# Kernel optimization log

Hardware: AMD Instinct MI355X
Metric: run time of the kernel (lower is better)

Reference implementation:

```python
import jax, jax.numpy as jnp
import numpy as np
from jax import lax

D_IN, HIDDEN, B, T = 64, 512, 256, 256


def _lstm_layer(x, W_ih, W_hh, b_ih, b_hh):
    """PyTorch-convention LSTM layer. x: [B, T, in]. Returns (ys [B,T,H], h_last [B,H]).
    Gate order i, f, g, o; gates = x W_ih^T + h W_hh^T + b_ih + b_hh."""
    Bb = x.shape[0]
    H = W_hh.shape[1]
    # precompute input projection for all timesteps: [T, B, 4H]
    xg = jnp.einsum('bti,gi->tbg', x, W_ih) + (b_ih + b_hh)
    h0 = jnp.zeros((Bb, H), dtype=x.dtype)
    c0 = jnp.zeros((Bb, H), dtype=x.dtype)

    def step(carry, xg_t):
        h, c = carry
        gates = xg_t + h @ W_hh.T  # [B, 4H]
        i, f, g, o = jnp.split(gates, 4, axis=-1)
        i = jax.nn.sigmoid(i)
        f = jax.nn.sigmoid(f)
        g = jnp.tanh(g)
        o = jax.nn.sigmoid(o)
        c = f * c + i * g
        h = o * jnp.tanh(c)
        return (h, c), h

    (h_last, _), ys = lax.scan(step, (h0, c0), xg)
    return ys.transpose(1, 0, 2), h_last


def setup_inputs() -> dict:
    key = jax.random.key(0)
    ks = jax.random.split(key, 12)
    s0 = 1.0 / np.sqrt(HIDDEN)  # PyTorch default init scale
    u = lambda k, shp: jax.random.uniform(k, shp, jnp.float32, -s0, s0)
    return {
        'x': jax.random.normal(ks[0], (B, T, D_IN), jnp.float32),
        'W_ih0': u(ks[1], (4 * HIDDEN, D_IN)),
        'W_hh0': u(ks[2], (4 * HIDDEN, HIDDEN)),
        'b_ih0': u(ks[3], (4 * HIDDEN,)),
        'b_hh0': u(ks[4], (4 * HIDDEN,)),
        'W_ih1': u(ks[5], (4 * HIDDEN, HIDDEN)),
        'W_hh1': u(ks[6], (4 * HIDDEN, HIDDEN)),
        'b_ih1': u(ks[7], (4 * HIDDEN,)),
        'b_hh1': u(ks[8], (4 * HIDDEN,)),
        'head_w': u(ks[9], (1, HIDDEN)),
        'head_b': u(ks[10], (1,)),
    }


def reference(x, W_ih0, W_hh0, b_ih0, b_hh0, W_ih1, W_hh1, b_ih1, b_hh1, head_w, head_b):
    ys0, _ = _lstm_layer(x, W_ih0, W_hh0, b_ih0, b_hh0)          # [B, T, H]
    _, h_last = _lstm_layer(ys0, W_ih1, W_hh1, b_ih1, b_hh1)    # only last step used
    out = h_last @ head_w.T + head_b                              # [B, 1]
    return out[:, 0]                                              # squeeze(-1) -> [B]
```

## Files before the change

kernel.cpp:

```cpp
#include <hip/hip_runtime.h>

#define HID 512
#define NB  256
#define TT  256
#define DIN 64
#define HBUF 131072
#define SLOT_SH HBUF
#define NSLOT 8

typedef __attribute__((ext_vector_type(8))) short short8;
typedef __attribute__((ext_vector_type(4))) float f32x4;

__device__ __forceinline__ unsigned short f2bf(float f) {
    unsigned int u = __float_as_uint(f);
    u += 0x7FFF + ((u >> 16) & 1);
    return (unsigned short)(u >> 16);
}
__device__ __forceinline__ float bf2f(unsigned short h) {
    return __uint_as_float(((unsigned int)h) << 16);
}

__device__ __forceinline__ float fsig(float x) {
    return __builtin_amdgcn_rcpf(1.f + __expf(-x));
}
__device__ __forceinline__ float ftanh(float x) {
    return 1.f - 2.f * __builtin_amdgcn_rcpf(1.f + __expf(2.f * x));
}

__device__ __forceinline__ void st_u32_llc(unsigned* p, unsigned v) {
    asm volatile("global_store_dword %0, %1, off sc0 sc1" :: "v"(p), "v"(v) : "memory");
}
__device__ __forceinline__ unsigned ld_u32_llc(const unsigned* p) {
    unsigned v;
    asm volatile("global_load_dword %0, %1, off sc0 sc1\n\ts_waitcnt vmcnt(0)"
                 : "=v"(v) : "v"(p) : "memory");
    return v;
}

#define MFMA1(acc, a, b) acc = __builtin_amdgcn_mfma_f32_16x16x32_bf16(a, b, acc, 0, 0, 0)

#define SW0_F 36
#define SW1_F 64
#define SW0_N (SW0_F * 512)
#define SW1_N (SW1_F * 512)
#define LDS_BYTES ((SW0_N + SW1_N) * 2)

__device__ __forceinline__ void store_h_pair(unsigned short* buf, size_t hoff,
                                             unsigned short v, int l) {
    unsigned int hv = (unsigned int)v;
    unsigned int up = __shfl_down(hv, 1);
    if ((l & 1) == 0)
        st_u32_llc((unsigned*)(buf + hoff), hv | (up << 16));
}

__device__ __forceinline__ void flag_wait(unsigned* fset, int target) {
    if (threadIdx.x < 64) {
        unsigned* p = fset + threadIdx.x;
        while ((int)ld_u32_llc(p) < target) __builtin_amdgcn_s_sleep(1);
    }
    __syncthreads();
}

__device__ __forceinline__ void orbit_transpose(f32x4& v, int m) {
    { float a = (m & 1) ? v[0] : v[1]; float b = __shfl_xor(a, 4); if (m & 1) v[0] = b; else v[1] = b; }
    { float a = (m & 1) ? v[2] : v[3]; float b = __shfl_xor(a, 4); if (m & 1) v[2] = b; else v[3] = b; }
    { float a = (m & 2) ? v[0] : v[2]; float b = __shfl_xor(a, 8); if (m & 2) v[0] = b; else v[2] = b; }
    { float a = (m & 2) ? v[1] : v[3]; float b = __shfl_xor(a, 8); if (m & 2) v[1] = b; else v[3] = b; }
}

__global__ __launch_bounds__(512, 2) void lstm_persistent(
    const float* __restrict__ x,
    const float* __restrict__ Wih0, const float* __restrict__ Whh0,
    const float* __restrict__ bih0, const float* __restrict__ bhh0,
    const float* __restrict__ Wih1, const float* __restrict__ Whh1,
    const float* __restrict__ bih1, const float* __restrict__ bhh1,
    const float* __restrict__ headw, const float* __restrict__ headb,
    unsigned short* h0base, unsigned short* h1base,
    unsigned* gf, float* __restrict__ out)
{
    extern __shared__ unsigned short lds[];
    unsigned short* sW0 = lds;
    unsigned short* sW1 = lds + SW0_N;

    const int tid = threadIdx.x;
    const int l   = tid & 63;
    const int w   = tid >> 6;
    const int bt  = w >> 1;
    const int bf  = w & 1;
    const int bid = blockIdx.x;
    const int gq  = bid & 3;
    const int jb  = bid >> 2;

    unsigned* f0g = gf + gq * 64;
    unsigned* f1g = gf + 256 + gq * 64;

    const int r16 = l & 15;
    const int ko  = (l >> 4) * 8;
    {
        const int nrow = (r16 >> 2) * HID + jb * 8 + (r16 & 3);
        for (int fi = w; fi < SW0_F; fi += 8) {
            const int kt = fi >> 1, bf_ = fi & 1;
            const int n = nrow + bf_ * 4;
            const float* src = (kt < 2) ? (Wih0 + (size_t)n * DIN + kt * 32 + ko)
                                        : (Whh0 + (size_t)n * HID + (kt - 2) * 32 + ko);
            float v[8];
            *(float4*)&v[0] = *(const float4*)src;
            *(float4*)&v[4] = *(const float4*)(src + 4);
            union { unsigned short u[8]; uint4 q; } pb;
            #pragma unroll
            for (int e = 0; e < 8; ++e) pb.u[e] = f2bf(v[e]);
            *(uint4*)&sW0[fi * 512 + l * 8] = pb.q;
        }
        for (int fi = w; fi < SW1_F; fi += 8) {
            const int kt = fi >> 1, bf_ = fi & 1;
            const int n = nrow + bf_ * 4;
            const float* src = (kt < 16) ? (Wih1 + (size_t)n * HID + kt * 32 + ko)
                                         : (Whh1 + (size_t)n * HID + (kt - 16) * 32 + ko);
            float v[8];
            *(float4*)&v[0] = *(const float4*)src;
            *(float4*)&v[4] = *(const float4*)(src + 4);
            union { unsigned short u[8]; uint4 q; } pb;
            #pragma unroll
            for (int e = 0; e < 8; ++e) pb.u[e] = f2bf(v[e]);
            *(uint4*)&sW1[fi * 512 + l * 8] = pb.q;
        }
    }

    float bias0[4], bias1[4];
    #pragma unroll
    for (int gi = 0; gi < 4; ++gi) {
        const int nn = gi * HID + jb * 8 + bf * 4 + (l & 3);
        bias0[gi] = bih0[nn] + bhh0[nn];
        bias1[gi] = bih1[nn] + bhh1[nn];
    }
    float c0 = 0.f, c1 = 0.f;

    const int m      = (l >> 2) & 3;
    const int b_in   = (l >> 4) * 4 + m;
    const int b_glob = gq * 64 + bt * 16 + b_in;
    const int j_glob = jb * 8 + bf * 4 + (l & 3);
    const size_t hoff = ((((size_t)(b_glob >> 4)) * 16 + (j_glob >> 5)) * 64
                         + ((b_glob & 15) | (((j_glob >> 3) & 3) << 4))) * 8 + (j_glob & 7);
    const int btg = gq * 4 + bt;

    const int xrow = gq * 64 + bt * 16 + (l & 15);
    float xv0[8], xv1[8];
    {
        const float* s0 = x + ((size_t)xrow * TT + 0) * DIN + ko;
        *(float4*)&xv0[0] = *(const float4*)s0;
        *(float4*)&xv0[4] = *(const float4*)(s0 + 4);
        *(float4*)&xv1[0] = *(const float4*)(s0 + 32);
        *(float4*)&xv1[4] = *(const float4*)(s0 + 36);
    }

    __syncthreads();

    const short8 bx0 = *(const short8*)&sW0[(0 * 2 + bf) * 512 + l * 8];
    const short8 bx1 = *(const short8*)&sW0[(1 * 2 + bf) * 512 + l * 8];

    for (int it = 0; it <= TT; ++it) {
        flag_wait(f0g, it);

        const unsigned short* h0c = h0base + (size_t)((it + 7) & 7) * SLOT_SH;
        unsigned short* h0n       = h0base + (size_t)(it & 7) * SLOT_SH;
        const unsigned short* h1c = h1base + (size_t)((it + 6) & 7) * SLOT_SH;
        unsigned short* h1n       = h1base + (size_t)((it + 7) & 7) * SLOT_SH;

        f32x4 acc0[2] = {{0.f,0.f,0.f,0.f},{0.f,0.f,0.f,0.f}};
        f32x4 acc1[2] = {{0.f,0.f,0.f,0.f},{0.f,0.f,0.f,0.f}};

        short8 fAh[16];
        #pragma unroll
        for (int kt = 0; kt < 16; ++kt) {
            const size_t o = (((size_t)btg * 16 + kt) * 64 + l) * 8;
            fAh[kt] = *(const short8*)&h0c[o];
        }

        if (it < TT) {
            {
                union { unsigned short u[8]; short8 s; } ah, al;
                #pragma unroll
                for (int e = 0; e < 8; ++e) {
                    unsigned short h = f2bf(xv0[e]);
                    ah.u[e] = h; al.u[e] = f2bf(xv0[e] - bf2f(h));
                }
                MFMA1(acc0[0], ah.s, bx0);
                MFMA1(acc0[0], al.s, bx0);
                #pragma unroll
                for (int e = 0; e < 8; ++e) {
                    unsigned short h = f2bf(xv1[e]);
                    ah.u[e] = h; al.u[e] = f2bf(xv1[e] - bf2f(h));
                }
                MFMA1(acc0[1], ah.s, bx1);
                MFMA1(acc0[1], al.s, bx1);
            }
            #pragma unroll
            for (int kt = 0; kt < 16; ++kt) {
                short8 b = *(const short8*)&sW0[((kt + 2) * 2 + bf) * 512 + l * 8];
                MFMA1(acc0[kt & 1], fAh[kt], b);
            }
            {
                f32x4 v = acc0[0] + acc0[1];
                orbit_transpose(v, m);
                const float iG = fsig(v[0] + bias0[0]);
                const float fG = fsig(v[1] + bias0[1]);
                const float gT = ftanh(v[2] + bias0[2]);
                const float oG = fsig(v[3] + bias0[3]);
                c0 = fmaf(fG, c0, iG * gT);
                const float h = oG * ftanh(c0);
                store_h_pair(h0n, hoff, f2bf(h), l);
            }
            asm volatile("s_waitcnt vmcnt(0)" ::: "memory");
            __syncthreads();
            if (tid == 0) st_u32_llc(f0g + jb, (unsigned)(it + 1));
        }

        if (it + 1 < TT) {
            const float* s0 = x + ((size_t)xrow * TT + (it + 1)) * DIN + ko;
            *(float4*)&xv0[0] = *(const float4*)s0;
            *(float4*)&xv0[4] = *(const float4*)(s0 + 4);
            *(float4*)&xv1[0] = *(const float4*)(s0 + 32);
            *(float4*)&xv1[4] = *(const float4*)(s0 + 36);
        }

        if (it > 0) {
            #pragma unroll
            for (int kt = 0; kt < 16; ++kt) {
                short8 b = *(const short8*)&sW1[(kt * 2 + bf) * 512 + l * 8];
                MFMA1(acc1[kt & 1], fAh[kt], b);
            }
        }

        flag_wait(f1g, it);

        if (it > 0) {
            short8 fCh[16];
            #pragma unroll
            for (int kt = 0; kt < 16; ++kt) {
                const size_t o = (((size_t)btg * 16 + kt) * 64 + l) * 8;
                fCh[kt] = *(const short8*)&h1c[o];
            }
            #pragma unroll
            for (int kt = 0; kt < 16; ++kt) {
                short8 b = *(const short8*)&sW1[((16 + kt) * 2 + bf) * 512 + l * 8];
                MFMA1(acc1[kt & 1], fCh[kt], b);
            }
            {
                f32x4 v = acc1[0] + acc1[1];
                orbit_transpose(v, m);
                const float iG = fsig(v[0] + bias1[0]);
                const float fG = fsig(v[1] + bias1[1]);
                const float gT = ftanh(v[2] + bias1[2]);
                const float oG = fsig(v[3] + bias1[3]);
                c1 = fmaf(fG, c1, iG * gT);
                const float h = oG * ftanh(c1);
                store_h_pair(h1n, hoff, f2bf(h), l);
            }
        }
        asm volatile("s_waitcnt vmcnt(0)" ::: "memory");
        __syncthreads();
        if (tid == 0) st_u32_llc(f1g + jb, (unsigned)(it + 1));
        if ((it & 7) == 7 && tid >= 448)
            __builtin_amdgcn_fence(__ATOMIC_ACQUIRE, "agent");
    }

    if (jb == 0) {
        if (tid < 64) {
            unsigned* p = f1g + tid;
            while ((int)ld_u32_llc(p) < TT + 1) __builtin_amdgcn_s_sleep(1);
        }
        __syncthreads();
        const unsigned short* h1h = h1base + (size_t)((TT + 7) & 7) * SLOT_SH;
        const int bl_ = tid >> 3;
        const int qd  = tid & 7;
        const int b   = gq * 64 + bl_;
        const int btw = b >> 4;
        float s = 0.f;
        #pragma unroll
        for (int jt = qd * 2; jt < qd * 2 + 2; ++jt) {
            #pragma unroll
            for (int q2 = 0; q2 < 4; ++q2) {
                const size_t off = (((size_t)btw * 16 + jt) * 64 + ((b & 15) | (q2 << 4))) * 8;
                short8 vh = *(const short8*)&h1h[off];
                const int j0 = jt * 32 + q2 * 8;
                #pragma unroll
                for (int e = 0; e < 8; ++e)
                    s += bf2f((unsigned short)vh[e]) * headw[j0 + e];
            }
        }
        s += __shfl_down(s, 4, 8);
        s += __shfl_down(s, 2, 8);
        s += __shfl_down(s, 1, 8);
        if (qd == 0) out[b] = s + headb[0];
    }
}

extern "C" void kernel_launch(void* const* d_in, const int* in_sizes, int n_in,
                              void* d_out, int out_size, void* d_ws, size_t ws_size,
                              hipStream_t stream) {
    const float* x      = (const float*)d_in[0];
    const float* W_ih0  = (const float*)d_in[1];
    const float* W_hh0  = (const float*)d_in[2];
    const float* b_ih0  = (const float*)d_in[3];
    const float* b_hh0  = (const float*)d_in[4];
    const float* W_ih1  = (const float*)d_in[5];
    const float* W_hh1  = (const float*)d_in[6];
    const float* b_ih1  = (const float*)d_in[7];
    const float* b_hh1  = (const float*)d_in[8];
    const float* head_w = (const float*)d_in[9];
    const float* head_b = (const float*)d_in[10];
    float* out = (float*)d_out;

    const size_t SLOT_BYTES = (size_t)SLOT_SH * 2;
    unsigned* gf = (unsigned*)d_ws;
    unsigned short* h0base = (unsigned short*)((char*)d_ws + (1 << 20));
    unsigned short* h1base = (unsigned short*)((char*)d_ws + (1 << 20) + NSLOT * SLOT_BYTES);

    hipMemsetAsync(d_ws, 0, 4096, stream);
    hipMemsetAsync((char*)h0base + 7 * SLOT_BYTES, 0, SLOT_BYTES, stream);
    hipMemsetAsync((char*)h1base + 7 * SLOT_BYTES, 0, SLOT_BYTES, stream);

    hipFuncSetAttribute((const void*)lstm_persistent,
                        hipFuncAttributeMaxDynamicSharedMemorySize, LDS_BYTES);
    lstm_persistent<<<dim3(256), dim3(512), LDS_BYTES, stream>>>(
        x, W_ih0, W_hh0, b_ih0, b_hh0, W_ih1, W_hh1, b_ih1, b_hh1,
        head_w, head_b, h0base, h1base, gf, out);
}
```

Baseline: 1.450 ms.

## Replace block-wide barriers with per-wave cohort flag synchronization

Each wave now waits on and publishes its own flags, keyed to its batch-tile cohort and gate half, instead of the block doing __syncthreads and a single block-level flag per step. This removes two block barriers per timestep and lets waves in the same block progress independently. Only waves that share the same rows of the hidden state wait on each other. It also adds a periodic barrier plus fence every 8 steps to bound how far waves drift apart. The cost is 64 lanes polling two flag arrays per wave, more flag traffic, and a larger flag area (16 KB memset).

```diff
diff --git a/kernel.cpp b/kernel.cpp
--- a/kernel.cpp
+++ b/kernel.cpp
@@ -53,12 +53,11 @@
         st_u32_llc((unsigned*)(buf + hoff), hv | (up << 16));
 }
 
-__device__ __forceinline__ void flag_wait(unsigned* fset, int target) {
-    if (threadIdx.x < 64) {
-        unsigned* p = fset + threadIdx.x;
-        while ((int)ld_u32_llc(p) < target) __builtin_amdgcn_s_sleep(1);
-    }
-    __syncthreads();
+__device__ __forceinline__ void cohort_wait(unsigned* fc, int l, int target) {
+    unsigned* pa = fc + l;
+    unsigned* pb = fc + 64 + l;
+    while ((int)ld_u32_llc(pa) < target) __builtin_amdgcn_s_sleep(1);
+    while ((int)ld_u32_llc(pb) < target) __builtin_amdgcn_s_sleep(1);
 }
 
 __device__ __forceinline__ void orbit_transpose(f32x4& v, int m) {
@@ -91,8 +90,11 @@
     const int gq  = bid & 3;
     const int jb  = bid >> 2;
 
-    unsigned* f0g = gf + gq * 64;
-    unsigned* f1g = gf + 256 + gq * 64;
+    const int cohort = gq * 4 + bt;
+    unsigned* f0c = gf + cohort * 128;
+    unsigned* f1c = gf + 2048 + cohort * 128;
+    unsigned* f0sig = f0c + bf * 64 + jb;
+    unsigned* f1sig = f1c + bf * 64 + jb;
 
     const int r16 = l & 15;
     const int ko  = (l >> 4) * 8;
@@ -159,7 +161,7 @@
     const short8 bx1 = *(const short8*)&sW0[(1 * 2 + bf) * 512 + l * 8];
 
     for (int it = 0; it <= TT; ++it) {
-        flag_wait(f0g, it);
+        cohort_wait(f0c, l, it);
 
         const unsigned short* h0c = h0base + (size_t)((it + 7) & 7) * SLOT_SH;
         unsigned short* h0n       = h0base + (size_t)(it & 7) * SLOT_SH;
@@ -211,8 +213,7 @@
                 store_h_pair(h0n, hoff, f2bf(h), l);
             }
             asm volatile("s_waitcnt vmcnt(0)" ::: "memory");
-            __syncthreads();
-            if (tid == 0) st_u32_llc(f0g + jb, (unsigned)(it + 1));
+            if (l == 0) st_u32_llc(f0sig, (unsigned)(it + 1));
         }
 
         if (it + 1 < TT) {
@@ -231,7 +232,7 @@
             }
         }
 
-        flag_wait(f1g, it);
+        cohort_wait(f1c, l, it);
 
         if (it > 0) {
             short8 fCh[16];
@@ -258,16 +259,20 @@
             }
         }
         asm volatile("s_waitcnt vmcnt(0)" ::: "memory");
-        __syncthreads();
-        if (tid == 0) st_u32_llc(f1g + jb, (unsigned)(it + 1));
-        if ((it & 7) == 7 && tid >= 448)
-            __builtin_amdgcn_fence(__ATOMIC_ACQUIRE, "agent");
+        if (l == 0) st_u32_llc(f1sig, (unsigned)(it + 1));
+
+        if ((it & 7) == 7) {
+            __syncthreads();
+            if (tid >= 448)
+                __builtin_amdgcn_fence(__ATOMIC_ACQUIRE, "agent");
+            __syncthreads();
+        }
     }
 
     if (jb == 0) {
-        if (tid < 64) {
-            unsigned* p = f1g + tid;
-            while ((int)ld_u32_llc(p) < TT + 1) __builtin_amdgcn_s_sleep(1);
+        {
+            unsigned* hp = gf + 2048 + gq * 512 + tid;
+            while ((int)ld_u32_llc(hp) < TT + 1) __builtin_amdgcn_s_sleep(1);
         }
         __syncthreads();
         const unsigned short* h1h = h1base + (size_t)((TT + 7) & 7) * SLOT_SH;
@@ -316,7 +321,7 @@
     unsigned short* h0base = (unsigned short*)((char*)d_ws + (1 << 20));
     unsigned short* h1base = (unsigned short*)((char*)d_ws + (1 << 20) + NSLOT * SLOT_BYTES);
 
-    hipMemsetAsync(d_ws, 0, 4096, stream);
+    hipMemsetAsync(d_ws, 0, 16384, stream);
     hipMemsetAsync((char*)h0base + 7 * SLOT_BYTES, 0, SLOT_BYTES, stream);
     hipMemsetAsync((char*)h1base + 7 * SLOT_BYTES, 0, SLOT_BYTES, stream);
 
```

Result: slower. 1.545 ms (+6.5%).
